# Performance work log

Hardware: AMD Instinct MI355X
Metric: run time of the kernel (lower is better)

The kernel has to match this reference:

```python
import jax, jax.numpy as jnp
import numpy as np

N_NODES = 100000
N_EDGES = 3200000
NUM_FEATURES = 256
HIDDEN = 16
NUM_CLASSES = 40


def gcn_conv(x, edge_index, W, b, num_nodes):
    """PyG GCNConv: linear -> add self-loops -> symmetric deg norm -> scatter-add -> bias."""
    x = x @ W  # [N, out]
    loop = jnp.arange(num_nodes)
    src = jnp.concatenate([edge_index[0], loop])  # messages flow src -> dst
    dst = jnp.concatenate([edge_index[1], loop])
    # degree of target nodes (with self-loops)
    deg = jax.ops.segment_sum(jnp.ones_like(dst, dtype=x.dtype), dst,
                              num_segments=num_nodes)
    dinv = jnp.where(deg > 0, jax.lax.rsqrt(deg), 0.0)
    norm = dinv[src] * dinv[dst]  # [E+N]
    out = jax.ops.segment_sum(x[src] * norm[:, None], dst,
                              num_segments=num_nodes)
    return out + b


def setup_inputs() -> dict:
    key = jax.random.key(0)
    k1, k2, k3, k4 = jax.random.split(key, 4)
    x = jax.random.normal(k1, (N_NODES, NUM_FEATURES), dtype=jnp.float32)
    edge_index = jax.random.randint(k2, (2, N_EDGES), 0, N_NODES, dtype=jnp.int64)
    W1 = jax.random.normal(k3, (NUM_FEATURES, HIDDEN), dtype=jnp.float32) / np.sqrt(NUM_FEATURES)
    b1 = jnp.zeros((HIDDEN,), dtype=jnp.float32)
    W2 = jax.random.normal(k4, (HIDDEN, NUM_CLASSES), dtype=jnp.float32) / np.sqrt(HIDDEN)
    b2 = jnp.zeros((NUM_CLASSES,), dtype=jnp.float32)
    return {"x": x, "edge_index": edge_index, "W1": W1, "b1": b1, "W2": W2, "b2": b2}


def reference(x, edge_index, W1, b1, W2, b2):
    h = jax.nn.relu(gcn_conv(x, edge_index, W1, b1, N_NODES))
    return gcn_conv(h, edge_index, W2, b2, N_NODES)
```

## Files before the change

kernel.cpp:

```cpp
#include <hip/hip_runtime.h>
#include <hip/hip_fp16.h>

#define N_NODES   100000
#define N_EDGES   3200000
#define F_IN      256
#define HID       16
#define NCLS      40

#define CHUNK     16384
#define NBLK      ((N_EDGES + CHUNK - 1) / CHUNK)
#define B2SHIFT   9
#define NB2       ((N_NODES + 511) >> B2SHIFT)
#define BCAP      17408

__global__ __launch_bounds__(256) void hist_kernel(const int* __restrict__ ei,
                                                   int* __restrict__ hist_blk) {
    __shared__ int h[NB2];
    int blk = blockIdx.x, t = threadIdx.x;
    for (int i = t; i < NB2; i += 256) h[i] = 0;
    __syncthreads();
    int e0 = blk * CHUNK;
    int eN = min(CHUNK, N_EDGES - e0);
    for (int i = t; i < eN; i += 256)
        atomicAdd(&h[ei[N_EDGES + e0 + i] >> B2SHIFT], 1);
    __syncthreads();
    for (int i = t; i < NB2; i += 256) hist_blk[i * NBLK + blk] = h[i];
}

__global__ __launch_bounds__(256) void rowscan_kernel(int* __restrict__ hist_blk,
                                                      int* __restrict__ rowsum) {
    __shared__ int part[256];
    int b = blockIdx.x, t = threadIdx.x;
    int v = (t < NBLK) ? hist_blk[b * NBLK + t] : 0;
    part[t] = v;
    __syncthreads();
    for (int off = 1; off < 256; off <<= 1) {
        int u = (t >= off) ? part[t - off] : 0;
        __syncthreads();
        part[t] += u;
        __syncthreads();
    }
    if (t < NBLK) hist_blk[b * NBLK + t] = part[t] - v;
    if (t == 255) rowsum[b] = part[255];
}

__global__ __launch_bounds__(256) void basescan_kernel(const int* __restrict__ rowsum,
                                                       int* __restrict__ bucket_base) {
    __shared__ int part[256];
    int t = threadIdx.x;
    int v = (t < NB2) ? rowsum[t] : 0;
    part[t] = v;
    __syncthreads();
    for (int off = 1; off < 256; off <<= 1) {
        int u = (t >= off) ? part[t - off] : 0;
        __syncthreads();
        part[t] += u;
        __syncthreads();
    }
    if (t < NB2) bucket_base[t] = part[t] - v;
}

__global__ __launch_bounds__(256) void bin2_kernel(const int* __restrict__ ei,
                                                   const int* __restrict__ hist_blk,
                                                   const int* __restrict__ bucket_base,
                                                   int* __restrict__ buf) {
    __shared__ int cur[NB2];
    int blk = blockIdx.x, t = threadIdx.x;
    for (int i = t; i < NB2; i += 256)
        cur[i] = bucket_base[i] + hist_blk[i * NBLK + blk];
    __syncthreads();
    int e0 = blk * CHUNK;
    int eN = min(CHUNK, N_EDGES - e0);
    for (int i = t; i < eN; i += 256) {
        int d = ei[N_EDGES + e0 + i];
        int s = ei[e0 + i];
        int pos = atomicAdd(&cur[d >> B2SHIFT], 1);
        buf[pos] = ((d & 511) << 17) | s;
    }
}

__global__ __launch_bounds__(512) void build_kernel(const int* __restrict__ buf,
                                                    const int* __restrict__ bucket_base,
                                                    const int* __restrict__ rowsum,
                                                    int* __restrict__ rowptr,
                                                    float* __restrict__ dinv,
                                                    int* __restrict__ csr_src) {
    __shared__ int lbuf[BCAP];
    __shared__ int hist[512], offs[512], cur[512];
    int b = blockIdx.x, t = threadIdx.x;
    int base = bucket_base[b];
    int cnt  = rowsum[b];
    hist[t] = 0;
    __syncthreads();
    for (int i = t; i < cnt; i += 512) {
        int v = buf[base + i];
        if (i < BCAP) lbuf[i] = v;
        atomicAdd(&hist[v >> 17], 1);
    }
    __syncthreads();
    int v = hist[t];
    offs[t] = v;
    __syncthreads();
    for (int off = 1; off < 512; off <<= 1) {
        int u = (t >= off) ? offs[t - off] : 0;
        __syncthreads();
        offs[t] += u;
        __syncthreads();
    }
    int ex = offs[t] - v;
    int n = (b << B2SHIFT) + t;
    if (n < N_NODES) {
        rowptr[n] = base + ex;
        dinv[n]   = rsqrtf((float)(v + 1));
    }
    if (b == 0 && t == 0) rowptr[N_NODES] = N_EDGES;
    cur[t] = ex;
    __syncthreads();
    for (int i = t; i < cnt; i += 512) {
        int p = (i < BCAP) ? lbuf[i] : buf[base + i];
        int pos = atomicAdd(&cur[p >> 17], 1);
        csr_src[base + pos] = p & 0x1FFFF;
    }
}

__global__ __launch_bounds__(256) void gemm1_kernel(const float* __restrict__ x,
                                                    const float* __restrict__ W1,
                                                    const float* __restrict__ dinv,
                                                    __half* __restrict__ y1h) {
    __shared__ float W1s[F_IN * HID];
    int t = threadIdx.x;
    #pragma unroll
    for (int i = 0; i < (F_IN * HID) / 256; i++) W1s[t + i * 256] = W1[t + i * 256];
    __syncthreads();

    int n = blockIdx.x * 256 + t;
    if (n >= N_NODES) return;

    const float4* xr = (const float4*)(x + (size_t)n * F_IN);
    float acc[HID];
    #pragma unroll
    for (int h = 0; h < HID; h++) acc[h] = 0.f;

    #pragma unroll 4
    for (int k4 = 0; k4 < F_IN / 4; k4++) {
        float4 xv = xr[k4];
        int k = k4 * 4;
        #pragma unroll
        for (int h = 0; h < HID; h++) {
            acc[h] += xv.x * W1s[(k + 0) * HID + h] + xv.y * W1s[(k + 1) * HID + h]
                    + xv.z * W1s[(k + 2) * HID + h] + xv.w * W1s[(k + 3) * HID + h];
        }
    }
    float dv = dinv[n];
    __half2 hp[8];
    #pragma unroll
    for (int j = 0; j < 8; j++)
        hp[j] = __float22half2_rn(make_float2(acc[2 * j] * dv, acc[2 * j + 1] * dv));
    float4* o = (float4*)(y1h + (size_t)n * HID);
    o[0] = ((float4*)hp)[0];
    o[1] = ((float4*)hp)[1];
}

__device__ __forceinline__ void acc_row(const float4* __restrict__ tab, int s, float* acc) {
    float4 v0 = tab[(size_t)s * 2 + 0];
    float4 v1 = tab[(size_t)s * 2 + 1];
    const __half2* a0 = (const __half2*)&v0;
    const __half2* a1 = (const __half2*)&v1;
    #pragma unroll
    for (int j = 0; j < 4; j++) {
        float2 f0 = __half22float2(a0[j]);
        float2 f1 = __half22float2(a1[j]);
        acc[2 * j]         += f0.x;
        acc[2 * j + 1]     += f0.y;
        acc[8 + 2 * j]     += f1.x;
        acc[8 + 2 * j + 1] += f1.y;
    }
}

__global__ __launch_bounds__(256) void gather1_kernel(const int* __restrict__ rowptr,
                                                      const int* __restrict__ csr_src,
                                                      const __half* __restrict__ y1h,
                                                      const float* __restrict__ b1,
                                                      const float* __restrict__ dinv,
                                                      __half* __restrict__ zh) {
    int n   = blockIdx.x * 16 + (threadIdx.x >> 4);
    int sub = threadIdx.x & 15;
    const float4* tab = (const float4*)y1h;
    int beg = rowptr[n], end = rowptr[n + 1];
    float acc[16];
    #pragma unroll
    for (int i = 0; i < 16; i++) acc[i] = 0.f;
    if (sub == 0) acc_row(tab, n, acc);
    for (int e = beg + sub; e < end; e += 16)
        acc_row(tab, csr_src[e], acc);
    #pragma unroll
    for (int m = 1; m < 16; m <<= 1) {
        #pragma unroll
        for (int i = 0; i < 16; i++) acc[i] += __shfl_xor(acc[i], m, 16);
    }
    if (sub < 2) {
        float dv = dinv[n];
        const float4* b1q = (const float4*)b1;
        float4 ba = b1q[sub * 2], bb = b1q[sub * 2 + 1];
        const float* bp = (sub == 0) ? (const float*)&ba : (const float*)&ba;
        float bv[8] = {ba.x, ba.y, ba.z, ba.w, bb.x, bb.y, bb.z, bb.w};
        (void)bp;
        __half2 outp[4];
        #pragma unroll
        for (int j = 0; j < 4; j++) {
            float2 r;
            r.x = fmaxf(dv * acc[sub * 8 + 2 * j]     + bv[2 * j],     0.f) * dv;
            r.y = fmaxf(dv * acc[sub * 8 + 2 * j + 1] + bv[2 * j + 1], 0.f) * dv;
            outp[j] = __float22half2_rn(r);
        }
        *(float4*)(zh + (size_t)n * HID + sub * 8) = *(float4*)outp;
    }
}

__global__ __launch_bounds__(256) void gather2_kernel(const int* __restrict__ rowptr,
                                                      const int* __restrict__ csr_src,
                                                      const __half* __restrict__ zh,
                                                      const float* __restrict__ W2,
                                                      const float* __restrict__ b2,
                                                      const float* __restrict__ dinv,
                                                      float* __restrict__ out) {
    __shared__ float W2s[HID * NCLS];
    __shared__ float b2s[NCLS];
    int t = threadIdx.x;
    for (int i = t; i < HID * NCLS; i += 256) W2s[i] = W2[i];
    if (t < NCLS) b2s[t] = b2[t];
    __syncthreads();

    int n   = blockIdx.x * 16 + (t >> 4);
    int sub = t & 15;
    const float4* tab = (const float4*)zh;
    int beg = rowptr[n], end = rowptr[n + 1];
    float acc[16];
    #pragma unroll
    for (int i = 0; i < 16; i++) acc[i] = 0.f;
    if (sub == 0) acc_row(tab, n, acc);
    for (int e = beg + sub; e < end; e += 16)
        acc_row(tab, csr_src[e], acc);
    #pragma unroll
    for (int m = 1; m < 16; m <<= 1) {
        #pragma unroll
        for (int i = 0; i < 16; i++) acc[i] += __shfl_xor(acc[i], m, 16);
    }
    if (sub < 10) {
        float dv = dinv[n];
        int c0 = sub * 4;
        float o0 = 0.f, o1 = 0.f, o2 = 0.f, o3 = 0.f;
        #pragma unroll
        for (int h = 0; h < HID; h++) {
            float a = acc[h];
            const float* w = &W2s[h * NCLS + c0];
            o0 += a * w[0]; o1 += a * w[1]; o2 += a * w[2]; o3 += a * w[3];
        }
        float4 r = make_float4(dv * o0 + b2s[c0],     dv * o1 + b2s[c0 + 1],
                               dv * o2 + b2s[c0 + 2], dv * o3 + b2s[c0 + 3]);
        *(float4*)(out + (size_t)n * NCLS + c0) = r;
    }
}

extern "C" void kernel_launch(void* const* d_in, const int* in_sizes, int n_in,
                              void* d_out, int out_size, void* d_ws, size_t ws_size,
                              hipStream_t stream) {
    const float* x   = (const float*)d_in[0];
    const int*   ei  = (const int*)  d_in[1];
    const float* W1  = (const float*)d_in[2];
    const float* b1  = (const float*)d_in[3];
    const float* W2  = (const float*)d_in[4];
    const float* b2  = (const float*)d_in[5];
    float* out = (float*)d_out;

    char* ws = (char*)d_ws;
    size_t off = 0;
    int*   hist_blk    = (int*)(ws + off); off += (size_t)NB2 * NBLK * 4;
    int*   rowsum      = (int*)(ws + off); off += (size_t)NB2 * 4;
    int*   bucket_base = (int*)(ws + off); off += (size_t)NB2 * 4;
    off = (off + 15) & ~(size_t)15;
    int*    rowptr  = (int*)   (ws + off); off += (size_t)(N_NODES + 1) * 4;
    off = (off + 15) & ~(size_t)15;
    float*  dinv    = (float*) (ws + off); off += (size_t)N_NODES * 4;
    int*    csr_src = (int*)   (ws + off); off += (size_t)N_EDGES * 4;
    int*    buf     = (int*)   (ws + off); off += (size_t)N_EDGES * 4;
    __half* y1h     = (__half*)(ws + off); off += (size_t)N_NODES * HID * 2;
    __half* zh      = (__half*)(ws + off); off += (size_t)N_NODES * HID * 2;

    hist_kernel    <<<NBLK, 256, 0, stream>>>(ei, hist_blk);
    rowscan_kernel <<<NB2, 256, 0, stream>>>(hist_blk, rowsum);
    basescan_kernel<<<1, 256, 0, stream>>>(rowsum, bucket_base);
    bin2_kernel    <<<NBLK, 256, 0, stream>>>(ei, hist_blk, bucket_base, buf);
    build_kernel   <<<NB2, 512, 0, stream>>>(buf, bucket_base, rowsum, rowptr, dinv, csr_src);

    gemm1_kernel  <<<(N_NODES + 255) / 256, 256, 0, stream>>>(x, W1, dinv, y1h);
    gather1_kernel<<<N_NODES / 16, 256, 0, stream>>>(rowptr, csr_src, y1h, b1, dinv, zh);
    gather2_kernel<<<N_NODES / 16, 256, 0, stream>>>(rowptr, csr_src, zh, W2, b2, dinv, out);
}
```

Measured before the change: 357.9 us.

## Vectorize edge loads, fold base scan into consumers, two nodes per GEMM thread

The histogram and binning kernels now read edge indices as int4 vectors. The separate single-block base scan is removed, and each bin2 and build block recomputes the bucket prefix sum itself. gemm1 computes two nodes per thread so each W1 shared-memory read is reused, and the gather kernels unroll the neighbor loop by two to keep more loads in flight. The changes cut one launch and some memory and shared-memory traffic, but they add redundant scan work per block, raise register pressure, and halve the GEMM grid.

Result: faster. 327.7 us (-8.4%).

```diff
diff --git a/kernel.cpp b/kernel.cpp
--- a/kernel.cpp
+++ b/kernel.cpp
@@ -21,8 +21,14 @@
     __syncthreads();
     int e0 = blk * CHUNK;
     int eN = min(CHUNK, N_EDGES - e0);
-    for (int i = t; i < eN; i += 256)
-        atomicAdd(&h[ei[N_EDGES + e0 + i] >> B2SHIFT], 1);
+    const int4* d4 = (const int4*)(ei + N_EDGES + e0);
+    for (int i = t; i < (eN >> 2); i += 256) {
+        int4 d = d4[i];
+        atomicAdd(&h[d.x >> B2SHIFT], 1);
+        atomicAdd(&h[d.y >> B2SHIFT], 1);
+        atomicAdd(&h[d.z >> B2SHIFT], 1);
+        atomicAdd(&h[d.w >> B2SHIFT], 1);
+    }
     __syncthreads();
     for (int i = t; i < NB2; i += 256) hist_blk[i * NBLK + blk] = h[i];
 }
@@ -44,54 +50,58 @@
     if (t == 255) rowsum[b] = part[255];
 }
 
-__global__ __launch_bounds__(256) void basescan_kernel(const int* __restrict__ rowsum,
-                                                       int* __restrict__ bucket_base) {
-    __shared__ int part[256];
-    int t = threadIdx.x;
-    int v = (t < NB2) ? rowsum[t] : 0;
-    part[t] = v;
-    __syncthreads();
-    for (int off = 1; off < 256; off <<= 1) {
-        int u = (t >= off) ? part[t - off] : 0;
-        __syncthreads();
-        part[t] += u;
-        __syncthreads();
-    }
-    if (t < NB2) bucket_base[t] = part[t] - v;
-}
-
 __global__ __launch_bounds__(256) void bin2_kernel(const int* __restrict__ ei,
                                                    const int* __restrict__ hist_blk,
-                                                   const int* __restrict__ bucket_base,
+                                                   const int* __restrict__ rowsum,
                                                    int* __restrict__ buf) {
     __shared__ int cur[NB2];
+    __shared__ int sc[256];
     int blk = blockIdx.x, t = threadIdx.x;
-    for (int i = t; i < NB2; i += 256)
-        cur[i] = bucket_base[i] + hist_blk[i * NBLK + blk];
+    int rv = (t < NB2) ? rowsum[t] : 0;
+    sc[t] = rv;
+    __syncthreads();
+    for (int off = 1; off < 256; off <<= 1) {
+        int u = (t >= off) ? sc[t - off] : 0;
+        __syncthreads();
+        sc[t] += u;
+        __syncthreads();
+    }
+    if (t < NB2) cur[t] = (sc[t] - rv) + hist_blk[t * NBLK + blk];
     __syncthreads();
     int e0 = blk * CHUNK;
     int eN = min(CHUNK, N_EDGES - e0);
-    for (int i = t; i < eN; i += 256) {
-        int d = ei[N_EDGES + e0 + i];
-        int s = ei[e0 + i];
-        int pos = atomicAdd(&cur[d >> B2SHIFT], 1);
-        buf[pos] = ((d & 511) << 17) | s;
+    const int4* s4 = (const int4*)(ei + e0);
+    const int4* d4 = (const int4*)(ei + N_EDGES + e0);
+    for (int i = t; i < (eN >> 2); i += 256) {
+        int4 d = d4[i], s = s4[i];
+        int p0 = atomicAdd(&cur[d.x >> B2SHIFT], 1); buf[p0] = ((d.x & 511) << 17) | s.x;
+        int p1 = atomicAdd(&cur[d.y >> B2SHIFT], 1); buf[p1] = ((d.y & 511) << 17) | s.y;
+        int p2 = atomicAdd(&cur[d.z >> B2SHIFT], 1); buf[p2] = ((d.z & 511) << 17) | s.z;
+        int p3 = atomicAdd(&cur[d.w >> B2SHIFT], 1); buf[p3] = ((d.w & 511) << 17) | s.w;
     }
 }
 
 __global__ __launch_bounds__(512) void build_kernel(const int* __restrict__ buf,
-                                                    const int* __restrict__ bucket_base,
                                                     const int* __restrict__ rowsum,
                                                     int* __restrict__ rowptr,
                                                     float* __restrict__ dinv,
                                                     int* __restrict__ csr_src) {
     __shared__ int lbuf[BCAP];
     __shared__ int hist[512], offs[512], cur[512];
+    __shared__ int sc[256];
     int b = blockIdx.x, t = threadIdx.x;
-    int base = bucket_base[b];
+    int rv = 0;
+    if (t < 256) { rv = (t < NB2) ? rowsum[t] : 0; sc[t] = rv; }
+    hist[t] = 0;
+    __syncthreads();
+    for (int off = 1; off < 256; off <<= 1) {
+        int u = (t < 256 && t >= off) ? sc[t - off] : 0;
+        __syncthreads();
+        if (t < 256) sc[t] += u;
+        __syncthreads();
+    }
     int cnt  = rowsum[b];
-    hist[t] = 0;
-    __syncthreads();
+    int base = sc[b] - cnt;
     for (int i = t; i < cnt; i += 512) {
         int v = buf[base + i];
         if (i < BCAP) lbuf[i] = v;
@@ -133,32 +143,52 @@
     for (int i = 0; i < (F_IN * HID) / 256; i++) W1s[t + i * 256] = W1[t + i * 256];
     __syncthreads();
 
-    int n = blockIdx.x * 256 + t;
-    if (n >= N_NODES) return;
-
-    const float4* xr = (const float4*)(x + (size_t)n * F_IN);
-    float acc[HID];
-    #pragma unroll
-    for (int h = 0; h < HID; h++) acc[h] = 0.f;
-
-    #pragma unroll 4
+    int n0 = blockIdx.x * 512 + t;
+    int n1 = n0 + 256;
+    if (n0 >= N_NODES) return;
+    bool v1 = (n1 < N_NODES);
+
+    const float4* xr0 = (const float4*)(x + (size_t)n0 * F_IN);
+    const float4* xr1 = (const float4*)(x + (size_t)(v1 ? n1 : n0) * F_IN);
+    float acc0[HID], acc1[HID];
+    #pragma unroll
+    for (int h = 0; h < HID; h++) { acc0[h] = 0.f; acc1[h] = 0.f; }
+
+    #pragma unroll 2
     for (int k4 = 0; k4 < F_IN / 4; k4++) {
-        float4 xv = xr[k4];
+        float4 xa = xr0[k4];
+        float4 xb = xr1[k4];
         int k = k4 * 4;
         #pragma unroll
         for (int h = 0; h < HID; h++) {
-            acc[h] += xv.x * W1s[(k + 0) * HID + h] + xv.y * W1s[(k + 1) * HID + h]
-                    + xv.z * W1s[(k + 2) * HID + h] + xv.w * W1s[(k + 3) * HID + h];
+            float w0 = W1s[(k + 0) * HID + h];
+            float w1 = W1s[(k + 1) * HID + h];
+            float w2 = W1s[(k + 2) * HID + h];
+            float w3 = W1s[(k + 3) * HID + h];
+            acc0[h] += xa.x * w0 + xa.y * w1 + xa.z * w2 + xa.w * w3;
+            acc1[h] += xb.x * w0 + xb.y * w1 + xb.z * w2 + xb.w * w3;
         }
     }
-    float dv = dinv[n];
-    __half2 hp[8];
-    #pragma unroll
-    for (int j = 0; j < 8; j++)
-        hp[j] = __float22half2_rn(make_float2(acc[2 * j] * dv, acc[2 * j + 1] * dv));
-    float4* o = (float4*)(y1h + (size_t)n * HID);
-    o[0] = ((float4*)hp)[0];
-    o[1] = ((float4*)hp)[1];
+    {
+        float dv = dinv[n0];
+        __half2 hp[8];
+        #pragma unroll
+        for (int j = 0; j < 8; j++)
+            hp[j] = __float22half2_rn(make_float2(acc0[2 * j] * dv, acc0[2 * j + 1] * dv));
+        float4* o = (float4*)(y1h + (size_t)n0 * HID);
+        o[0] = ((float4*)hp)[0];
+        o[1] = ((float4*)hp)[1];
+    }
+    if (v1) {
+        float dv = dinv[n1];
+        __half2 hp[8];
+        #pragma unroll
+        for (int j = 0; j < 8; j++)
+            hp[j] = __float22half2_rn(make_float2(acc1[2 * j] * dv, acc1[2 * j + 1] * dv));
+        float4* o = (float4*)(y1h + (size_t)n1 * HID);
+        o[0] = ((float4*)hp)[0];
+        o[1] = ((float4*)hp)[1];
+    }
 }
 
 __device__ __forceinline__ void acc_row(const float4* __restrict__ tab, int s, float* acc) {
@@ -174,6 +204,28 @@
         acc[2 * j + 1]     += f0.y;
         acc[8 + 2 * j]     += f1.x;
         acc[8 + 2 * j + 1] += f1.y;
+    }
+}
+
+__device__ __forceinline__ void acc_row2(const float4* __restrict__ tab, int s0, int s1, float* acc) {
+    float4 v0 = tab[(size_t)s0 * 2 + 0];
+    float4 v1 = tab[(size_t)s0 * 2 + 1];
+    float4 v2 = tab[(size_t)s1 * 2 + 0];
+    float4 v3 = tab[(size_t)s1 * 2 + 1];
+    const __half2* a0 = (const __half2*)&v0;
+    const __half2* a1 = (const __half2*)&v1;
+    const __half2* b0 = (const __half2*)&v2;
+    const __half2* b1 = (const __half2*)&v3;
+    #pragma unroll
+    for (int j = 0; j < 4; j++) {
+        float2 f0 = __half22float2(a0[j]);
+        float2 f1 = __half22float2(a1[j]);
+        float2 g0 = __half22float2(b0[j]);
+        float2 g1 = __half22float2(b1[j]);
+        acc[2 * j]         += f0.x + g0.x;
+        acc[2 * j + 1]     += f0.y + g0.y;
+        acc[8 + 2 * j]     += f1.x + g1.x;
+        acc[8 + 2 * j + 1] += f1.y + g1.y;
     }
 }
 
@@ -191,8 +243,10 @@
     #pragma unroll
     for (int i = 0; i < 16; i++) acc[i] = 0.f;
     if (sub == 0) acc_row(tab, n, acc);
-    for (int e = beg + sub; e < end; e += 16)
-        acc_row(tab, csr_src[e], acc);
+    int e = beg + sub;
+    for (; e + 16 < end; e += 32)
+        acc_row2(tab, csr_src[e], csr_src[e + 16], acc);
+    if (e < end) acc_row(tab, csr_src[e], acc);
     #pragma unroll
     for (int m = 1; m < 16; m <<= 1) {
         #pragma unroll
@@ -202,9 +256,7 @@
         float dv = dinv[n];
         const float4* b1q = (const float4*)b1;
         float4 ba = b1q[sub * 2], bb = b1q[sub * 2 + 1];
-        const float* bp = (sub == 0) ? (const float*)&ba : (const float*)&ba;
         float bv[8] = {ba.x, ba.y, ba.z, ba.w, bb.x, bb.y, bb.z, bb.w};
-        (void)bp;
         __half2 outp[4];
         #pragma unroll
         for (int j = 0; j < 4; j++) {
@@ -239,8 +291,10 @@
     #pragma unroll
     for (int i = 0; i < 16; i++) acc[i] = 0.f;
     if (sub == 0) acc_row(tab, n, acc);
-    for (int e = beg + sub; e < end; e += 16)
-        acc_row(tab, csr_src[e], acc);
+    int e = beg + sub;
+    for (; e + 16 < end; e += 32)
+        acc_row2(tab, csr_src[e], csr_src[e + 16], acc);
+    if (e < end) acc_row(tab, csr_src[e], acc);
     #pragma unroll
     for (int m = 1; m < 16; m <<= 1) {
         #pragma unroll
@@ -275,9 +329,8 @@
 
     char* ws = (char*)d_ws;
     size_t off = 0;
-    int*   hist_blk    = (int*)(ws + off); off += (size_t)NB2 * NBLK * 4;
-    int*   rowsum      = (int*)(ws + off); off += (size_t)NB2 * 4;
-    int*   bucket_base = (int*)(ws + off); off += (size_t)NB2 * 4;
+    int*   hist_blk = (int*)(ws + off); off += (size_t)NB2 * NBLK * 4;
+    int*   rowsum   = (int*)(ws + off); off += (size_t)NB2 * 4;
     off = (off + 15) & ~(size_t)15;
     int*    rowptr  = (int*)   (ws + off); off += (size_t)(N_NODES + 1) * 4;
     off = (off + 15) & ~(size_t)15;
@@ -289,11 +342,10 @@
 
     hist_kernel    <<<NBLK, 256, 0, stream>>>(ei, hist_blk);
     rowscan_kernel <<<NB2, 256, 0, stream>>>(hist_blk, rowsum);
-    basescan_kernel<<<1, 256, 0, stream>>>(rowsum, bucket_base);
-    bin2_kernel    <<<NBLK, 256, 0, stream>>>(ei, hist_blk, bucket_base, buf);
-    build_kernel   <<<NB2, 512, 0, stream>>>(buf, bucket_base, rowsum, rowptr, dinv, csr_src);
-
-    gemm1_kernel  <<<(N_NODES + 255) / 256, 256, 0, stream>>>(x, W1, dinv, y1h);
+    bin2_kernel    <<<NBLK, 256, 0, stream>>>(ei, hist_blk, rowsum, buf);
+    build_kernel   <<<NB2, 512, 0, stream>>>(buf, rowsum, rowptr, dinv, csr_src);
+
+    gemm1_kernel  <<<(N_NODES + 511) / 512, 256, 0, stream>>>(x, W1, dinv, y1h);
     gather1_kernel<<<N_NODES / 16, 256, 0, stream>>>(rowptr, csr_src, y1h, b1, dinv, zh);
     gather2_kernel<<<N_NODES / 16, 256, 0, stream>>>(rowptr, csr_src, zh, W2, b2, dinv, out);
 }
```
